# Kernel optimization log

Hardware: AMD Instinct MI355X
Metric: run time of the kernel (lower is better)

## Reference

```python
import jax, jax.numpy as jnp
import numpy as np

N_NODES = 100000


def gcn_conv(x, src, dst, W, b, num_nodes):
    # PyG GCNConv: add self-loops, symmetric normalization D^-1/2 (A+I) D^-1/2, then linear.
    loop = jnp.arange(num_nodes, dtype=src.dtype)
    s = jnp.concatenate([src, loop])
    d = jnp.concatenate([dst, loop])
    deg = jax.ops.segment_sum(jnp.ones_like(d, dtype=x.dtype), d, num_segments=num_nodes)
    dinv = jnp.where(deg > 0, jax.lax.rsqrt(deg), 0.0)
    norm = dinv[s] * dinv[d]                       # [E+N]
    h = x @ W                                      # [N, out]
    msg = h[s] * norm[:, None]                     # gather + scale
    out = jax.ops.segment_sum(msg, d, num_segments=num_nodes)  # scatter-add
    return out + b


def setup_inputs() -> dict:
    key = jax.random.key(0)
    k1, k2, k3, k4 = jax.random.split(key, 4)
    F_IN, HID, C = 165, 128, 2
    E = 3200000
    x = jax.random.normal(k1, (N_NODES, F_IN), dtype=jnp.float32)
    edge_index = jax.random.randint(k2, (2, E), 0, N_NODES, dtype=jnp.int64)
    W1 = jax.random.normal(k3, (F_IN, HID), dtype=jnp.float32) * (1.0 / np.sqrt(F_IN))
    b1 = jnp.zeros((HID,), dtype=jnp.float32)
    W2 = jax.random.normal(k4, (HID, C), dtype=jnp.float32) * (1.0 / np.sqrt(HID))
    b2 = jnp.zeros((C,), dtype=jnp.float32)
    return {"x": x, "edge_index": edge_index, "W1": W1, "b1": b1, "W2": W2, "b2": b2}


def reference(x, edge_index, W1, b1, W2, b2):
    src, dst = edge_index[0], edge_index[1]
    h = jax.nn.relu(gcn_conv(x, src, dst, W1, b1, N_NODES))
    # dropout is identity in eval mode (self.training=False)
    out = gcn_conv(h, src, dst, W2, b2, N_NODES)
    return out
```

## Files before the change

kernel.cpp:

```cpp
#include <hip/hip_runtime.h>

#define NN  100000
#define FIN 165
#define HID 128
#define NBUCK 391
#define CHUNK 8192
#define KPAD 192
#define BH_STRIDE 400
#define XS 36

typedef __attribute__((ext_vector_type(4))) float f32x4;
typedef __attribute__((ext_vector_type(8))) short short8;

#define OFF_DINV   0
#define OFF_H1     100352
#define OFF_Z      (OFF_H1 + NN * 64)
#define OFF_ROWPTR (OFF_Z + 2 * NN)
#define OFF_GCNT   (OFF_ROWPTR + 100352)
#define OFF_GBASE  (OFF_GCNT + 512)
#define OFF_GCUR   (OFF_GBASE + 512)
#define OFF_BUCK   (OFF_GCUR + 512)
#define OFF_EDATA  (OFF_BUCK + 3200000)
#define OFF_WTHI   (OFF_EDATA + 3200000)
#define OFF_BHIST  (OFF_WTHI + 12288)

__device__ __forceinline__ unsigned bf16rne(float f) {
    unsigned u = __float_as_uint(f);
    return (u + 0x7FFFu + ((u >> 16) & 1u)) >> 16;
}

__device__ __forceinline__ float2 bf2_to_f2(unsigned int u) {
    float2 r;
    r.x = __uint_as_float(u << 16);
    r.y = __uint_as_float(u & 0xffff0000u);
    return r;
}

__device__ __forceinline__ short8 ldfrag(const ushort* p) {
    union { uint2 u[2]; short8 s; } f;
    f.u[0] = *(const uint2*)p;
    f.u[1] = *(const uint2*)(p + 16);
    return f.s;
}

__global__ void k_wsplit(const float* __restrict__ W1, ushort* __restrict__ hi,
                         int* __restrict__ gcnt) {
    int t = blockIdx.x * blockDim.x + threadIdx.x;
    if (t < 512) gcnt[t] = 0;
    if (t >= HID * KPAD) return;
    int ch = t / KPAD, k = t % KPAD;
    float v = (k < FIN) ? W1[k * HID + ch] : 0.0f;
    hi[ch * KPAD + k] = (ushort)bf16rne(v);
}

__global__ __launch_bounds__(256) void k_bcount(const int* __restrict__ dst,
        int* __restrict__ gcnt, int* __restrict__ bhist, int ne) {
    __shared__ int hist[NBUCK];
    for (int i = threadIdx.x; i < NBUCK; i += 256) hist[i] = 0;
    __syncthreads();
    const int4* dst4 = (const int4*)dst;
    const int ne4 = ne >> 2;
    const int base4 = blockIdx.x * (CHUNK / 4);
#pragma unroll
    for (int it = 0; it < CHUNK / 1024; ++it) {
        int e4 = base4 + it * 256 + threadIdx.x;
        if (e4 < ne4) {
            int4 v = dst4[e4];
            atomicAdd(&hist[v.x >> 8], 1);
            atomicAdd(&hist[v.y >> 8], 1);
            atomicAdd(&hist[v.z >> 8], 1);
            atomicAdd(&hist[v.w >> 8], 1);
        }
    }
    if (blockIdx.x == 0 && threadIdx.x < (ne & 3))
        atomicAdd(&hist[dst[(ne & ~3) + threadIdx.x] >> 8], 1);
    __syncthreads();
    int* brow = bhist + (size_t)blockIdx.x * BH_STRIDE;
    for (int i = threadIdx.x; i < NBUCK; i += 256) {
        int h = hist[i];
        brow[i] = h;
        if (h) atomicAdd(&gcnt[i], h);
    }
}

__global__ __launch_bounds__(512) void k_bscan(const int* __restrict__ gcnt,
        int* __restrict__ gbase, int* __restrict__ gcur, int ne) {
    __shared__ int s[512];
    int tid = threadIdx.x;
    int v = (tid < NBUCK) ? gcnt[tid] : 0;
    s[tid] = v;
    __syncthreads();
    for (int off = 1; off < 512; off <<= 1) {
        int t = (tid >= off) ? s[tid - off] : 0;
        __syncthreads();
        s[tid] += t;
        __syncthreads();
    }
    if (tid < NBUCK) {
        int ex = s[tid] - v;
        gbase[tid] = ex;
        gcur[tid] = ex;
    }
    if (tid == 0) gbase[NBUCK] = ne;
}

__global__ __launch_bounds__(256) void k_bfill(const int* __restrict__ src,
        const int* __restrict__ dst, int* __restrict__ gcur,
        const int* __restrict__ bhist, unsigned int* __restrict__ bucketed, int ne) {
    __shared__ int lcur[NBUCK];
    const int* brow = bhist + (size_t)blockIdx.x * BH_STRIDE;
    for (int i = threadIdx.x; i < NBUCK; i += 256) {
        int h = brow[i];
        lcur[i] = h ? atomicAdd(&gcur[i], h) : 0;
    }
    __syncthreads();
    const int4* dst4 = (const int4*)dst;
    const int4* src4 = (const int4*)src;
    const int ne4 = ne >> 2;
    const int base4 = blockIdx.x * (CHUNK / 4);
#pragma unroll
    for (int it = 0; it < CHUNK / 1024; ++it) {
        int e4 = base4 + it * 256 + threadIdx.x;
        if (e4 < ne4) {
            int4 d4 = dst4[e4];
            int4 s4 = src4[e4];
            int pos;
            pos = atomicAdd(&lcur[d4.x >> 8], 1);
            bucketed[pos] = (unsigned)s4.x | ((unsigned)(d4.x & 255) << 24);
            pos = atomicAdd(&lcur[d4.y >> 8], 1);
            bucketed[pos] = (unsigned)s4.y | ((unsigned)(d4.y & 255) << 24);
            pos = atomicAdd(&lcur[d4.z >> 8], 1);
            bucketed[pos] = (unsigned)s4.z | ((unsigned)(d4.z & 255) << 24);
            pos = atomicAdd(&lcur[d4.w >> 8], 1);
            bucketed[pos] = (unsigned)s4.w | ((unsigned)(d4.w & 255) << 24);
        }
    }
    if (blockIdx.x == 0 && threadIdx.x < (ne & 3)) {
        int e = (ne & ~3) + threadIdx.x;
        int d = dst[e];
        int pos = atomicAdd(&lcur[d >> 8], 1);
        bucketed[pos] = (unsigned)src[e] | ((unsigned)(d & 255) << 24);
    }
}

__global__ __launch_bounds__(256) void k_fine(const int* __restrict__ gbase,
        const unsigned int* __restrict__ bucketed, int* __restrict__ edata,
        int* __restrict__ rowptr, float* __restrict__ dinv, int n, int ne) {
    __shared__ int hist[256];
    __shared__ int scan[256];
    __shared__ int lcur[256];
    const int b = blockIdx.x;
    const int tid = threadIdx.x;
    const int beg = gbase[b], end = gbase[b + 1];
    hist[tid] = 0;
    __syncthreads();
    for (int j = beg + tid; j < end; j += 256)
        atomicAdd(&hist[bucketed[j] >> 24], 1);
    __syncthreads();
    int c = hist[tid];
    scan[tid] = c;
    __syncthreads();
    for (int off = 1; off < 256; off <<= 1) {
        int t = (tid >= off) ? scan[tid - off] : 0;
        __syncthreads();
        scan[tid] += t;
        __syncthreads();
    }
    int excl = scan[tid] - c;
    int d = b * 256 + tid;
    if (d < n) {
        rowptr[d] = beg + excl;
        dinv[d] = rsqrtf((float)c + 1.0f);
    }
    lcur[tid] = beg + excl;
    __syncthreads();
    for (int j = beg + tid; j < end; j += 256) {
        unsigned p = bucketed[j];
        int pos = atomicAdd(&lcur[p >> 24], 1);
        edata[pos] = (int)(p & 0x00FFFFFFu);
    }
    if (b == NBUCK - 1 && tid == 0) rowptr[n] = ne;
}

__global__ __launch_bounds__(256) void k_gemm1(const float* __restrict__ x,
        const ushort* __restrict__ wthi, unsigned* __restrict__ h1, int n) {
    __shared__ alignas(16) ushort xhi[64 * XS];
    __shared__ alignas(16) ushort whi[128 * XS];
    const int tid = threadIdx.x;
    const int node0 = blockIdx.x * 64;
    const int wv = tid >> 6, lane = tid & 63;
    const int r15 = lane & 15, g = lane >> 4;
    f32x4 acc[8];
#pragma unroll
    for (int ct = 0; ct < 8; ++ct) acc[ct] = (f32x4){0.f, 0.f, 0.f, 0.f};

    const int snd = tid >> 2, sq = tid & 3;
    const int sch = tid >> 1, sh = tid & 1;

    for (int ks = 0; ks < 6; ++ks) {
        {
            int gidx = sch * KPAD + ks * 32 + sh * 16;
            int lidx = sch * XS + sh * 16;
            uint4 a = *(const uint4*)&wthi[gidx];
            uint4 b = *(const uint4*)&wthi[gidx + 8];
            *(uint2*)&whi[lidx]      = make_uint2(a.x, a.y);
            *(uint2*)&whi[lidx + 4]  = make_uint2(a.z, a.w);
            *(uint2*)&whi[lidx + 8]  = make_uint2(b.x, b.y);
            *(uint2*)&whi[lidx + 12] = make_uint2(b.z, b.w);
        }
        {
            int node = node0 + snd;
            unsigned h8[8];
#pragma unroll
            for (int j = 0; j < 8; ++j) {
                int kk = ks * 32 + sq * 8 + j;
                float v = (node < n && kk < FIN) ? x[node * FIN + kk] : 0.0f;
                h8[j] = bf16rne(v);
            }
            int lidx = snd * XS + sq * 8;
            *(uint2*)&xhi[lidx]     = make_uint2(h8[0] | (h8[1] << 16), h8[2] | (h8[3] << 16));
            *(uint2*)&xhi[lidx + 4] = make_uint2(h8[4] | (h8[5] << 16), h8[6] | (h8[7] << 16));
        }
        __syncthreads();
        short8 Ah = ldfrag(&xhi[(wv * 16 + r15) * XS + 4 * g]);
#pragma unroll
        for (int ct = 0; ct < 8; ++ct) {
            short8 Bh = ldfrag(&whi[(ct * 16 + r15) * XS + 4 * g]);
            acc[ct] = __builtin_amdgcn_mfma_f32_16x16x32_bf16(Ah, Bh, acc[ct], 0, 0, 0);
        }
        __syncthreads();
    }
#pragma unroll
    for (int ct = 0; ct < 4; ++ct) {
#pragma unroll
        for (int r = 0; r < 4; ++r) {
            int node = node0 + wv * 16 + 4 * g + r;
            if (node < n) {
                unsigned p = bf16rne(acc[ct][r]) | (bf16rne(acc[ct + 4][r]) << 16);
                h1[node * 64 + ct * 16 + r15] = p;
            }
        }
    }
}

__global__ __launch_bounds__(256) void k_agg_fused(const int* __restrict__ rowptr,
        const int* __restrict__ edata, const unsigned int* __restrict__ h1,
        const float* __restrict__ dinv, const float* __restrict__ b1,
        const float* __restrict__ W2, float* __restrict__ z, int n0, int nn) {
    const int wid  = (blockIdx.x * blockDim.x + threadIdx.x) >> 6;
    const int lane = threadIdx.x & 63;
    if (wid >= nn) return;
    const int d = n0 + wid;
    const int beg = rowptr[d], end = rowptr[d + 1];
    const float di = dinv[d];
    const int grp = lane >> 4;
    const int sl  = lane & 15;

    float ax0, ax1, ax2, ax3, ay0, ay1, ay2, ay3;
    {
        uint4 hv = *(const uint4*)&h1[d * 64 + sl * 4];
        float nm = (grp == 0) ? di * di : 0.0f;
        float2 f0 = bf2_to_f2(hv.x), f1 = bf2_to_f2(hv.y);
        float2 f2 = bf2_to_f2(hv.z), f3 = bf2_to_f2(hv.w);
        ax0 = f0.x * nm; ay0 = f0.y * nm;
        ax1 = f1.x * nm; ay1 = f1.y * nm;
        ax2 = f2.x * nm; ay2 = f2.y * nm;
        ax3 = f3.x * nm; ay3 = f3.y * nm;
    }

#define PRELOAD(JB)                                                          \
    {                                                                        \
        int i0 = (JB) + grp, i1 = (JB) + 4 + grp,                            \
            i2 = (JB) + 8 + grp, i3 = (JB) + 12 + grp;                       \
        int c0 = min(i0, end - 1), c1 = min(i1, end - 1);                    \
        int c2 = min(i2, end - 1), c3 = min(i3, end - 1);                    \
        s0 = edata[c0]; s1 = edata[c1]; s2 = edata[c2]; s3 = edata[c3];      \
        m0 = (i0 < end) ? dinv[s0] * di : 0.0f;                              \
        m1 = (i1 < end) ? dinv[s1] * di : 0.0f;                              \
        m2 = (i2 < end) ? dinv[s2] * di : 0.0f;                              \
        m3 = (i3 < end) ? dinv[s3] * di : 0.0f;                              \
    }
#define ACC(G, NM)                                                           \
    {                                                                        \
        float2 f;                                                            \
        f = bf2_to_f2((G).x); ax0 = fmaf(f.x, (NM), ax0); ay0 = fmaf(f.y, (NM), ay0); \
        f = bf2_to_f2((G).y); ax1 = fmaf(f.x, (NM), ax1); ay1 = fmaf(f.y, (NM), ay1); \
        f = bf2_to_f2((G).z); ax2 = fmaf(f.x, (NM), ax2); ay2 = fmaf(f.y, (NM), ay2); \
        f = bf2_to_f2((G).w); ax3 = fmaf(f.x, (NM), ax3); ay3 = fmaf(f.y, (NM), ay3); \
    }

    if (beg < end) {
        int s0, s1, s2, s3;
        float m0, m1, m2, m3;
        PRELOAD(beg);
        for (int j = beg; j < end; j += 16) {
            uint4 g0 = *(const uint4*)&h1[s0 * 64 + sl * 4];
            uint4 g1 = *(const uint4*)&h1[s1 * 64 + sl * 4];
            uint4 g2 = *(const uint4*)&h1[s2 * 64 + sl * 4];
            uint4 g3 = *(const uint4*)&h1[s3 * 64 + sl * 4];
            float w0 = m0, w1 = m1, w2 = m2, w3 = m3;
            int jn = j + 16;
            if (jn < end) PRELOAD(jn);
            ACC(g0, w0); ACC(g1, w1); ACC(g2, w2); ACC(g3, w3);
        }
    }
#undef PRELOAD
#undef ACC

    ax0 += __shfl_xor(ax0, 16, 64); ax0 += __shfl_xor(ax0, 32, 64);
    ax1 += __shfl_xor(ax1, 16, 64); ax1 += __shfl_xor(ax1, 32, 64);
    ax2 += __shfl_xor(ax2, 16, 64); ax2 += __shfl_xor(ax2, 32, 64);
    ax3 += __shfl_xor(ax3, 16, 64); ax3 += __shfl_xor(ax3, 32, 64);
    ay0 += __shfl_xor(ay0, 16, 64); ay0 += __shfl_xor(ay0, 32, 64);
    ay1 += __shfl_xor(ay1, 16, 64); ay1 += __shfl_xor(ay1, 32, 64);
    ay2 += __shfl_xor(ay2, 16, 64); ay2 += __shfl_xor(ay2, 32, 64);
    ay3 += __shfl_xor(ay3, 16, 64); ay3 += __shfl_xor(ay3, 32, 64);
    const int c = sl * 4;
    float4 bA = *(const float4*)&b1[c];
    float4 bB = *(const float4*)&b1[c + 64];
    float v00 = ax0 + bA.x; v00 = v00 > 0.f ? v00 : 0.f;
    float v01 = ax1 + bA.y; v01 = v01 > 0.f ? v01 : 0.f;
    float v02 = ax2 + bA.z; v02 = v02 > 0.f ? v02 : 0.f;
    float v03 = ax3 + bA.w; v03 = v03 > 0.f ? v03 : 0.f;
    float v10 = ay0 + bB.x; v10 = v10 > 0.f ? v10 : 0.f;
    float v11 = ay1 + bB.y; v11 = v11 > 0.f ? v11 : 0.f;
    float v12 = ay2 + bB.z; v12 = v12 > 0.f ? v12 : 0.f;
    float v13 = ay3 + bB.w; v13 = v13 > 0.f ? v13 : 0.f;
    float4 wA0 = *(const float4*)&W2[c * 2];
    float4 wA1 = *(const float4*)&W2[c * 2 + 4];
    float4 wB0 = *(const float4*)&W2[(c + 64) * 2];
    float4 wB1 = *(const float4*)&W2[(c + 64) * 2 + 4];
    float p0 = v00 * wA0.x + v01 * wA0.z + v02 * wA1.x + v03 * wA1.z
             + v10 * wB0.x + v11 * wB0.z + v12 * wB1.x + v13 * wB1.z;
    float p1 = v00 * wA0.y + v01 * wA0.w + v02 * wA1.y + v03 * wA1.w
             + v10 * wB0.y + v11 * wB0.w + v12 * wB1.y + v13 * wB1.w;
#pragma unroll
    for (int m = 8; m >= 1; m >>= 1) {
        p0 += __shfl_xor(p0, m, 64);
        p1 += __shfl_xor(p1, m, 64);
    }
    if (lane == 0) *(float2*)&z[d * 2] = make_float2(p0, p1);
}

__global__ __launch_bounds__(256) void k_out(const int* __restrict__ rowptr,
        const int* __restrict__ edata, const float* __restrict__ z,
        const float* __restrict__ dinv, const float* __restrict__ b2,
        float* __restrict__ out, int n) {
    int g = (blockIdx.x * blockDim.x + threadIdx.x) >> 4;
    int l = threadIdx.x & 15;
    if (g >= n) return;
    int beg = rowptr[g], end = rowptr[g + 1];
    float di = dinv[g];
    float o0 = 0.0f, o1 = 0.0f;
    for (int j = beg + l; j < end; j += 16) {
        int s = edata[j];
        float nm = dinv[s] * di;
        float2 zs = *(const float2*)&z[s * 2];
        o0 = fmaf(zs.x, nm, o0);
        o1 = fmaf(zs.y, nm, o1);
    }
#pragma unroll
    for (int m = 8; m >= 1; m >>= 1) {
        o0 += __shfl_xor(o0, m, 16);
        o1 += __shfl_xor(o1, m, 16);
    }
    if (l == 0) {
        float2 zd = *(const float2*)&z[g * 2];
        float s2 = di * di;
        out[g * 2]     = fmaf(zd.x, s2, b2[0]) + o0;
        out[g * 2 + 1] = fmaf(zd.y, s2, b2[1]) + o1;
    }
}

extern "C" void kernel_launch(void* const* d_in, const int* in_sizes, int n_in,
                              void* d_out, int out_size, void* d_ws, size_t ws_size,
                              hipStream_t stream) {
    const float* x  = (const float*)d_in[0];
    const int*   ei = (const int*)d_in[1];
    const float* W1 = (const float*)d_in[2];
    const float* b1 = (const float*)d_in[3];
    const float* W2 = (const float*)d_in[4];
    const float* b2 = (const float*)d_in[5];
    float* out = (float*)d_out;

    const int n  = in_sizes[0] / FIN;
    const int ne = in_sizes[1] / 2;
    const int* src = ei;
    const int* dst = ei + ne;

    float* ws     = (float*)d_ws;
    float* dinv   = ws + OFF_DINV;
    unsigned int* h1 = (unsigned int*)(ws + OFF_H1);
    float* z      = ws + OFF_Z;
    int*   rowptr = (int*)(ws + OFF_ROWPTR);
    int*   gcnt   = (int*)(ws + OFF_GCNT);
    int*   gbase  = (int*)(ws + OFF_GBASE);
    int*   gcur   = (int*)(ws + OFF_GCUR);
    unsigned int* bucketed = (unsigned int*)(ws + OFF_BUCK);
    int*   edata  = (int*)(ws + OFF_EDATA);
    ushort* wthi  = (ushort*)(ws + OFF_WTHI);
    int*   bhist  = (int*)(ws + OFF_BHIST);

    const int nchb = (ne + CHUNK - 1) / CHUNK;

    k_wsplit<<<(HID * KPAD + 255) / 256, 256, 0, stream>>>(W1, wthi, gcnt);
    k_bcount<<<nchb, 256, 0, stream>>>(dst, gcnt, bhist, ne);
    k_bscan<<<1, 512, 0, stream>>>(gcnt, gbase, gcur, ne);
    k_bfill<<<nchb, 256, 0, stream>>>(src, dst, gcur, bhist, bucketed, ne);
    k_fine<<<NBUCK, 256, 0, stream>>>(gbase, bucketed, edata, rowptr, dinv, n, ne);
    k_gemm1<<<(n + 63) / 64, 256, 0, stream>>>(x, wthi, h1, n);
    const int half = (n + 1) / 2;
    k_agg_fused<<<(half * 64 + 255) / 256, 256, 0, stream>>>(rowptr, edata, h1, dinv, b1, W2, z, 0, half);
    k_agg_fused<<<((n - half) * 64 + 255) / 256, 256, 0, stream>>>(rowptr, edata, h1, dinv, b1, W2, z, half, n - half);
    k_out<<<(n * 16 + 255) / 256, 256, 0, stream>>>(rowptr, edata, z, dinv, b2, out, n);
}
```

Measured before the change: 261.0 us.

## Preload all W1 tiles and double-buffer x staging in gemm1; split aggregation into four launches

The gemm1 kernel now loads all six K-slices of the bf16 W1 into shared memory up front. It double-buffers the x tile so the next slice's global loads and bf16 conversion overlap the current slice's MFMAs, which removes one barrier per iteration. The aggregation kernel is also split into four launches instead of two, probably to improve cache locality per launch. In exchange, shared memory per block grows (about 64KB), which may reduce occupancy, and there are two extra kernel launches.

```diff
diff --git a/kernel.cpp b/kernel.cpp
--- a/kernel.cpp
+++ b/kernel.cpp
@@ -184,8 +184,8 @@
 
 __global__ __launch_bounds__(256) void k_gemm1(const float* __restrict__ x,
         const ushort* __restrict__ wthi, unsigned* __restrict__ h1, int n) {
-    __shared__ alignas(16) ushort xhi[64 * XS];
-    __shared__ alignas(16) ushort whi[128 * XS];
+    __shared__ alignas(16) ushort whi[6 * 128 * XS];
+    __shared__ alignas(16) ushort xb[2 * 64 * XS];
     const int tid = threadIdx.x;
     const int node0 = blockIdx.x * 64;
     const int wv = tid >> 6, lane = tid & 63;
@@ -197,39 +197,48 @@
     const int snd = tid >> 2, sq = tid & 3;
     const int sch = tid >> 1, sh = tid & 1;
 
+#pragma unroll
     for (int ks = 0; ks < 6; ++ks) {
-        {
-            int gidx = sch * KPAD + ks * 32 + sh * 16;
-            int lidx = sch * XS + sh * 16;
-            uint4 a = *(const uint4*)&wthi[gidx];
-            uint4 b = *(const uint4*)&wthi[gidx + 8];
-            *(uint2*)&whi[lidx]      = make_uint2(a.x, a.y);
-            *(uint2*)&whi[lidx + 4]  = make_uint2(a.z, a.w);
-            *(uint2*)&whi[lidx + 8]  = make_uint2(b.x, b.y);
-            *(uint2*)&whi[lidx + 12] = make_uint2(b.z, b.w);
-        }
-        {
-            int node = node0 + snd;
-            unsigned h8[8];
-#pragma unroll
-            for (int j = 0; j < 8; ++j) {
-                int kk = ks * 32 + sq * 8 + j;
-                float v = (node < n && kk < FIN) ? x[node * FIN + kk] : 0.0f;
-                h8[j] = bf16rne(v);
-            }
-            int lidx = snd * XS + sq * 8;
-            *(uint2*)&xhi[lidx]     = make_uint2(h8[0] | (h8[1] << 16), h8[2] | (h8[3] << 16));
-            *(uint2*)&xhi[lidx + 4] = make_uint2(h8[4] | (h8[5] << 16), h8[6] | (h8[7] << 16));
-        }
-        __syncthreads();
-        short8 Ah = ldfrag(&xhi[(wv * 16 + r15) * XS + 4 * g]);
+        int gidx = sch * KPAD + ks * 32 + sh * 16;
+        int lidx = ks * (128 * XS) + sch * XS + sh * 16;
+        uint4 a = *(const uint4*)&wthi[gidx];
+        uint4 b = *(const uint4*)&wthi[gidx + 8];
+        *(uint2*)&whi[lidx]      = make_uint2(a.x, a.y);
+        *(uint2*)&whi[lidx + 4]  = make_uint2(a.z, a.w);
+        *(uint2*)&whi[lidx + 8]  = make_uint2(b.x, b.y);
+        *(uint2*)&whi[lidx + 12] = make_uint2(b.z, b.w);
+    }
+
+#define STAGE_X(KS, BUF)                                                     \
+    {                                                                        \
+        int node = node0 + snd;                                              \
+        unsigned h8[8];                                                      \
+        _Pragma("unroll")                                                    \
+        for (int j = 0; j < 8; ++j) {                                        \
+            int kk = (KS) * 32 + sq * 8 + j;                                 \
+            float v = (node < n && kk < FIN) ? x[node * FIN + kk] : 0.0f;    \
+            h8[j] = bf16rne(v);                                              \
+        }                                                                    \
+        int lidx = (BUF) * (64 * XS) + snd * XS + sq * 8;                    \
+        *(uint2*)&xb[lidx]     = make_uint2(h8[0] | (h8[1] << 16), h8[2] | (h8[3] << 16)); \
+        *(uint2*)&xb[lidx + 4] = make_uint2(h8[4] | (h8[5] << 16), h8[6] | (h8[7] << 16)); \
+    }
+
+    STAGE_X(0, 0);
+    __syncthreads();
+    for (int ks = 0; ks < 6; ++ks) {
+        if (ks < 5) STAGE_X(ks + 1, (ks + 1) & 1);
+        short8 Ah = ldfrag(&xb[(ks & 1) * (64 * XS) + (wv * 16 + r15) * XS + 4 * g]);
+        const ushort* wbase = &whi[ks * (128 * XS)];
 #pragma unroll
         for (int ct = 0; ct < 8; ++ct) {
-            short8 Bh = ldfrag(&whi[(ct * 16 + r15) * XS + 4 * g]);
+            short8 Bh = ldfrag(&wbase[(ct * 16 + r15) * XS + 4 * g]);
             acc[ct] = __builtin_amdgcn_mfma_f32_16x16x32_bf16(Ah, Bh, acc[ct], 0, 0, 0);
         }
         __syncthreads();
     }
+#undef STAGE_X
+
 #pragma unroll
     for (int ct = 0; ct < 4; ++ct) {
 #pragma unroll
@@ -409,8 +418,13 @@
     k_bfill<<<nchb, 256, 0, stream>>>(src, dst, gcur, bhist, bucketed, ne);
     k_fine<<<NBUCK, 256, 0, stream>>>(gbase, bucketed, edata, rowptr, dinv, n, ne);
     k_gemm1<<<(n + 63) / 64, 256, 0, stream>>>(x, wthi, h1, n);
-    const int half = (n + 1) / 2;
-    k_agg_fused<<<(half * 64 + 255) / 256, 256, 0, stream>>>(rowptr, edata, h1, dinv, b1, W2, z, 0, half);
-    k_agg_fused<<<((n - half) * 64 + 255) / 256, 256, 0, stream>>>(rowptr, edata, h1, dinv, b1, W2, z, half, n - half);
+    const int q = (n + 3) / 4;
+    for (int i = 0; i < 4; ++i) {
+        int n0 = i * q;
+        int nn = (n - n0 < q) ? (n - n0) : q;
+        if (nn > 0)
+            k_agg_fused<<<((size_t)nn * 64 + 255) / 256, 256, 0, stream>>>(
+                rowptr, edata, h1, dinv, b1, W2, z, n0, nn);
+    }
     k_out<<<(n * 16 + 255) / 256, 256, 0, stream>>>(rowptr, edata, z, dinv, b2, out, n);
 }
```

Result: slower. 276.2 us (+5.8%).
